# Kernel tuning notes

Measured on AMD Instinct MI355X. Metric: run time of the kernel, lower is better.

The kernel has to match this reference:

```python
import jax, jax.numpy as jnp
import numpy as np

B, LQ, NK, D, H, FF, NL = 32, 96, 2048, 384, 8, 1536, 6
DH = D // H
NFUT = 32
GOAL_S, GRASP_S = 2046, 2047  # goal=[2046,2047), grasp=[2047,2048) in k_cross and k_self


def rotary3d(xyz):
    # RotaryPositionEncoding3D: per-axis sinusoids, interleaved duplication, concat over x/y/z
    d3 = D // 3
    div = jnp.exp(jnp.arange(0, d3, 2, dtype=jnp.float32) * (-np.log(10000.0) / d3))  # [d3/2]
    ang = xyz[..., None] * div  # [B,N,3,d3/2]
    cos = jnp.repeat(jnp.cos(ang), 2, axis=-1)  # [B,N,3,d3] (f0,f0,f1,f1,...)
    sin = jnp.repeat(jnp.sin(ang), 2, axis=-1)
    b, n = xyz.shape[:2]
    return cos.reshape(b, n, D), sin.reshape(b, n, D)


def rope(x, cos, sin):
    x2 = jnp.stack([-x[..., 1::2], x[..., ::2]], axis=-1).reshape(x.shape)
    return x * cos + x2 * sin


def layernorm(x, g, b):
    m = jnp.mean(x, -1, keepdims=True)
    v = jnp.var(x, -1, keepdims=True)
    return (x - m) * jax.lax.rsqrt(v + 1e-5) * g + b


def attn_block(x, kv, qcos, qsin, kcos, ksin, t_feats, p):
    (aw, ab, wq_, bq_, wk_, bk_, wv_, bv_, wo_, bo_, g1, b1, fw1_, fb1_, fw2_, fb2_, g2, b2_) = p
    # AdaLN: time-conditioned scale/shift on the query stream
    mod = jax.nn.silu(t_feats) @ aw + ab  # [B,2D]
    scale, shift = jnp.split(mod, 2, axis=-1)
    xq = x * (1.0 + scale[:, None, :]) + shift[:, None, :]
    qp = rope(xq @ wq_ + bq_, qcos, qsin).reshape(B, -1, H, DH)
    kp = rope(kv @ wk_ + bk_, kcos, ksin).reshape(B, -1, H, DH)
    vp = (kv @ wv_ + bv_).reshape(B, -1, H, DH)
    att = jax.nn.softmax(jnp.einsum('bqhd,bkhd->bhqk', qp, kp) / np.sqrt(DH), axis=-1)
    o = jnp.einsum('bhqk,bkhd->bqhd', att, vp).reshape(B, -1, D) @ wo_ + bo_
    x = layernorm(x + o, g1, b1)  # post-norm (pre_norm=False), residual on un-modulated x
    f = jax.nn.relu(x @ fw1_ + fb1_) @ fw2_ + fb2_
    return layernorm(x + f, g2, b2_)


def mlp_head(x, w1, b1, w2, b2, w3, b3):
    h = jax.nn.relu(x @ w1 + b1)
    h = jax.nn.relu(h @ w2 + b2)
    return h @ w3 + b3


def _forward(q, k_cross, k_self, q_xyz, k_xyz, timesteps,
             t_w1, t_b1, t_w2, t_b2, type_emb,
             ada_w, ada_b, wq, bq, wk, bk, wv, bv, wo, bo,
             ln1_g, ln1_b, fw1, fb1, fw2, fb2, ln2_g, ln2_b,
             act_w1, act_b1, act_w2, act_b2, act_w3, act_b3,
             qf_w1, qf_b1, qf_w2, qf_b2, qf_w3, qf_b3,
             ob_w1, ob_b1, ob_w2, ob_b2, ob_w3, ob_b3):
    # SinusoidalPosEmb + MLP time embedding
    half = D // 2
    freqs = jnp.exp(jnp.arange(half, dtype=jnp.float32) * (-np.log(10000.0) / (half - 1)))
    a = timesteps[:, None] * freqs
    pe = jnp.concatenate([jnp.sin(a), jnp.cos(a)], axis=-1)
    t_feats = jax.nn.relu(pe @ t_w1 + t_b1) @ t_w2 + t_b2  # [B,D]

    qcos, qsin = rotary3d(q_xyz)
    kcos, ksin = rotary3d(k_xyz)
    scos = jnp.concatenate([kcos, qcos], axis=1)  # self layers: seq2_pos = cat(pcd, grasp)
    ssin = jnp.concatenate([ksin, qsin], axis=1)

    # type embeddings (conditions_only -> goal=id3, grasp=id4)
    kc = k_cross.at[:, GOAL_S:GOAL_S + 1].add(type_emb[3]).at[:, GRASP_S:GRASP_S + 1].add(type_emb[4])
    ksf = k_self.at[:, GOAL_S:GOAL_S + 1].add(type_emb[3]).at[:, GRASP_S:GRASP_S + 1].add(type_emb[4])

    x = q
    for i in range(NL):
        p = (ada_w[i], ada_b[i], wq[i], bq[i], wk[i], bk[i], wv[i], bv[i], wo[i], bo[i],
             ln1_g[i], ln1_b[i], fw1[i], fb1[i], fw2[i], fb2[i], ln2_g[i], ln2_b[i])
        if i < 2:  # cross_attn module (2 layers) over scene tokens
            x = attn_block(x, kc, qcos, qsin, kcos, ksin, t_feats, p)
        else:      # 4 shared attention layers over k_self
            x = attn_block(x, ksf, qcos, qsin, scos, ssin, t_feats, p)

    act = mlp_head(x[:, :NFUT], act_w1, act_b1, act_w2, act_b2, act_w3, act_b3)            # [B,32,31]
    qf = mlp_head(x[:, NFUT:2 * NFUT], qf_w1, qf_b1, qf_w2, qf_b2, qf_w3, qf_b3)           # [B,32,31]
    ob = mlp_head(x[:, 2 * NFUT:], ob_w1, ob_b1, ob_w2, ob_b2, ob_w3, ob_b3)               # [B,32,9]
    return jnp.concatenate([act, qf, ob], axis=-1)  # [B,32,71]


def setup_inputs():
    ks = iter(jax.random.split(jax.random.key(0), 80))
    def w(shape, s=0.02):
        return jax.random.normal(next(ks), shape, jnp.float32) * s
    inp = {
        'q': jax.random.normal(next(ks), (B, LQ, D), jnp.float32),
        'k_cross': jax.random.normal(next(ks), (B, NK, D), jnp.float32),
        'k_self': jax.random.normal(next(ks), (B, NK + LQ, D), jnp.float32),
        'q_xyz': jax.random.normal(next(ks), (B, LQ, 3), jnp.float32),
        'k_xyz': jax.random.normal(next(ks), (B, NK, 3), jnp.float32),
        'timesteps': jax.random.uniform(next(ks), (B,), jnp.float32) * 1000.0,
        't_w1': w((D, D)), 't_b1': jnp.zeros((D,)), 't_w2': w((D, D)), 't_b2': jnp.zeros((D,)),
        'type_emb': w((8, D)),
        'ada_w': w((NL, D, 2 * D)), 'ada_b': jnp.zeros((NL, 2 * D)),
        'wq': w((NL, D, D)), 'bq': jnp.zeros((NL, D)),
        'wk': w((NL, D, D)), 'bk': jnp.zeros((NL, D)),
        'wv': w((NL, D, D)), 'bv': jnp.zeros((NL, D)),
        'wo': w((NL, D, D)), 'bo': jnp.zeros((NL, D)),
        'ln1_g': jnp.ones((NL, D)), 'ln1_b': jnp.zeros((NL, D)),
        'fw1': w((NL, D, FF)), 'fb1': jnp.zeros((NL, FF)),
        'fw2': w((NL, FF, D)), 'fb2': jnp.zeros((NL, D)),
        'ln2_g': jnp.ones((NL, D)), 'ln2_b': jnp.zeros((NL, D)),
        'act_w1': w((D, D)), 'act_b1': jnp.zeros((D,)), 'act_w2': w((D, D)), 'act_b2': jnp.zeros((D,)),
        'act_w3': w((D, 31)), 'act_b3': jnp.zeros((31,)),
        'qf_w1': w((D, D)), 'qf_b1': jnp.zeros((D,)), 'qf_w2': w((D, D)), 'qf_b2': jnp.zeros((D,)),
        'qf_w3': w((D, 31)), 'qf_b3': jnp.zeros((31,)),
        'ob_w1': w((D, D)), 'ob_b1': jnp.zeros((D,)), 'ob_w2': w((D, D)), 'ob_b2': jnp.zeros((D,)),
        'ob_w3': w((D, 9)), 'ob_b3': jnp.zeros((9,)),
    }
    return inp


def reference(q, k_cross, k_self, q_xyz, k_xyz, timesteps,
              t_w1, t_b1, t_w2, t_b2, type_emb,
              ada_w, ada_b, wq, bq, wk, bk, wv, bv, wo, bo,
              ln1_g, ln1_b, fw1, fb1, fw2, fb2, ln2_g, ln2_b,
              act_w1, act_b1, act_w2, act_b2, act_w3, act_b3,
              qf_w1, qf_b1, qf_w2, qf_b2, qf_w3, qf_b3,
              ob_w1, ob_b1, ob_w2, ob_b2, ob_w3, ob_b3):
    return _forward(q, k_cross, k_self, q_xyz, k_xyz, timesteps,
                    t_w1, t_b1, t_w2, t_b2, type_emb,
                    ada_w, ada_b, wq, bq, wk, bk, wv, bv, wo, bo,
                    ln1_g, ln1_b, fw1, fb1, fw2, fb2, ln2_g, ln2_b,
                    act_w1, act_b1, act_w2, act_b2, act_w3, act_b3,
                    qf_w1, qf_b1, qf_w2, qf_b2, qf_w3, qf_b3,
                    ob_w1, ob_b1, ob_w2, ob_b2, ob_w3, ob_b3)
```

## Files before the change

kernel.cpp:

```cpp
#include <hip/hip_runtime.h>
#include <hip/hip_fp16.h>

#define B_   32
#define LQ_  96
#define NK_  2048
#define D_   384
#define H_   8
#define DH_  48
#define FF_  1536
#define MQ_  (B_*LQ_)
#define SATT 8

typedef float  f32x4  __attribute__((ext_vector_type(4)));
typedef __bf16 bf16x8 __attribute__((ext_vector_type(8)));

__device__ __forceinline__ unsigned short f2bf(float f) {
  union { float f; unsigned u; } v; v.f = f;
  unsigned r = v.u + 0x7fffu + ((v.u >> 16) & 1u);
  return (unsigned short)(r >> 16);
}

__device__ __forceinline__ void ld_g2l(const unsigned short* g, unsigned short* l) {
  __builtin_amdgcn_global_load_lds(
      (const __attribute__((address_space(1))) void*)g,
      (__attribute__((address_space(3))) void*)l, 16, 0, 0);
}

__global__ void time_embed_kernel(const float* __restrict__ ts,
                                  const float* __restrict__ w1, const float* __restrict__ b1,
                                  const float* __restrict__ w2, const float* __restrict__ b2,
                                  float* __restrict__ s_out) {
  int b = blockIdx.x, d = threadIdx.x;
  __shared__ float pe[384];
  __shared__ float h1[384];
  float t = ts[b];
  int dd = (d < 192) ? d : d - 192;
  float f = expf((float)dd * (-9.210340371976184f / 191.0f));
  float ang = t * f;
  pe[d] = (d < 192) ? sinf(ang) : cosf(ang);
  __syncthreads();
  float acc = b1[d];
  for (int k = 0; k < 384; ++k) acc += pe[k] * w1[k * 384 + d];
  h1[d] = fmaxf(acc, 0.f);
  __syncthreads();
  acc = b2[d];
  for (int k = 0; k < 384; ++k) acc += h1[k] * w2[k * 384 + d];
  s_out[b * 384 + d] = acc / (1.f + expf(-acc));
}

__global__ void adaln_mod_kernel(const float* __restrict__ s,
                                 const float* __restrict__ aw, const float* __restrict__ ab,
                                 float* __restrict__ mod) {
  int b = blockIdx.x, l = blockIdx.y, c = threadIdx.x;
  __shared__ float ss[384];
  if (c < 384) ss[c] = s[b * 384 + c];
  __syncthreads();
  float acc = ab[l * 768 + c];
  const float* w = aw + (long)l * 384 * 768;
  for (int k = 0; k < 384; ++k) acc += ss[k] * w[k * 768 + c];
  mod[((long)l * 32 + b) * 768 + c] = acc;
}

__global__ void rope_pack_kernel(const float* __restrict__ xyz, __half2* __restrict__ cs,
                                 int total, int N, int ldn, int noff) {
  for (int i = blockIdx.x * blockDim.x + threadIdx.x; i < total;
       i += gridDim.x * blockDim.x) {
    int p = i % 192;
    int n = (i / 192) % N;
    int b = i / (192 * N);
    int a = p >> 6, j = p & 63;
    float div = __expf((float)j * (-9.210340371976184f / 64.0f));
    float ang = xyz[((long)b * N + n) * 3 + a] * div;
    float sv, cv;
    __sincosf(ang, &sv, &cv);
    cs[((long)b * ldn + noff + n) * 192 + p] = __floats2half2_rn(cv, sv);
  }
}

__global__ void cast_type_kernel(const float* __restrict__ in, const float* __restrict__ temb,
                                 unsigned short* __restrict__ out, long total, int N) {
  for (long i = blockIdx.x * (long)blockDim.x + threadIdx.x; i < total;
       i += (long)gridDim.x * blockDim.x) {
    int d = (int)(i % 384);
    int n = (int)((i / 384) % N);
    float v = in[i];
    if (n == 2046) v += temb[3 * 384 + d];
    else if (n == 2047) v += temb[4 * 384 + d];
    out[i] = f2bf(v);
  }
}

__global__ void wtrans_kernel(const float* __restrict__ in, unsigned short* __restrict__ out,
                              long total, int K, int N, int LDN, int noff) {
  for (long i = blockIdx.x * (long)blockDim.x + threadIdx.x; i < total;
       i += (long)gridDim.x * blockDim.x) {
    long l = i / ((long)K * N);
    long rem = i - l * (long)K * N;
    int n = (int)(rem / K);
    int k = (int)(rem % K);
    out[(l * LDN + noff + n) * K + k] = f2bf(in[l * (long)K * N + (long)k * N + n]);
  }
}

__global__ void modx_kernel(const float* __restrict__ x, const float* __restrict__ modl,
                            unsigned short* __restrict__ xq) {
  int i = blockIdx.x * blockDim.x + threadIdx.x;
  if (i >= MQ_ * D_) return;
  int d = i % 384;
  int b = (i / 384) / 96;
  float sc = modl[b * 768 + d];
  float sh = modl[b * 768 + 384 + d];
  xq[i] = f2bf(x[i] * (1.f + sc) + sh);
}

#define EPI_RELU   1
#define EPI_F32    2
#define EPI_ROPE_Q 3
#define EPI_KV     4

template <int EPI, int TM, int XT, int PERM>
__global__ __launch_bounds__(256)
void gemm_bt(const unsigned short* __restrict__ A, const unsigned short* __restrict__ Bt,
             const float* __restrict__ biasK, const float* __restrict__ biasV,
             void* __restrict__ Cout, void* __restrict__ Cout2,
             int Nt, int K, const __half2* __restrict__ cs, int tabOff, int nPerRow) {
  __shared__ __align__(16) unsigned short As[3][TM * 32];
  __shared__ __align__(16) unsigned short Bs[3][128 * 32];
  int tid = threadIdx.x, lane = tid & 63, wid = tid >> 6;
  int wm = (wid >> 1) * (TM / 2), wn = (wid & 1) * 64;
  int bx, byi;
  if (XT > 0) {
    int id = blockIdx.x;
    int xcd = id & 7, slot = id >> 3;
    bx = slot % XT;
    byi = (slot / XT) * 8 + xcd;
  } else {
    bx = blockIdx.x; byi = blockIdx.y;
  }
  int bn = bx * 128;
  long bm = (long)byi * TM;
  int r0 = tid >> 2;
  int cg = ((tid & 3) + (tid >> 3)) & 3;
  int c0 = cg * 8;
  long ar0 = bm + r0, ar1 = bm + 64 + r0;
  if (PERM) {
    ar0 = (ar0 >> 5) * 96 + tabOff + (ar0 & 31);
    ar1 = (ar1 >> 5) * 96 + tabOff + (ar1 & 31);
  }
  const unsigned short* gA0 = A + ar0 * K + c0;
  const unsigned short* gA1 = A + ar1 * K + c0;
  const unsigned short* gB0 = Bt + (long)(bn + r0) * K + c0;
  const unsigned short* gB1 = Bt + (long)(bn + 64 + r0) * K + c0;
  f32x4 acc[TM / 32][4] = {};
  int nk = K >> 5;
  int la = lane & 15, lg8 = lane >> 4;
  auto stage = [&](int buf) {
    ld_g2l(gA0, &As[buf][tid * 8]);
    if (TM == 128) ld_g2l(gA1, &As[buf][2048 + tid * 8]);
    ld_g2l(gB0, &Bs[buf][tid * 8]);
    ld_g2l(gB1, &Bs[buf][2048 + tid * 8]);
    gA0 += 32; gA1 += 32; gB0 += 32; gB1 += 32;
  };
  int offA[TM / 32], offB[4];
#pragma unroll
  for (int i = 0; i < TM / 32; ++i) {
    int row = wm + i * 16 + la;
    offA[i] = row * 32 + ((lg8 - (row >> 1)) & 3) * 8;
  }
#pragma unroll
  for (int j = 0; j < 4; ++j) {
    int row = wn + j * 16 + la;
    offB[j] = row * 32 + ((lg8 - (row >> 1)) & 3) * 8;
  }
  stage(0);
  stage(1);
  for (int kc = 0; kc < nk; ++kc) {
    int cur = kc % 3;
    if (kc < nk - 1) {
      if (TM == 128) asm volatile("s_waitcnt vmcnt(4) lgkmcnt(0)" ::: "memory");
      else           asm volatile("s_waitcnt vmcnt(3) lgkmcnt(0)" ::: "memory");
    } else {
      asm volatile("s_waitcnt vmcnt(0) lgkmcnt(0)" ::: "memory");
    }
    asm volatile("s_barrier" ::: "memory");
    if (kc + 2 < nk) stage((kc + 2) % 3);
    const unsigned short* Ab = &As[cur][0];
    const unsigned short* Bb = &Bs[cur][0];
    bf16x8 af[TM / 32], bfr[4];
#pragma unroll
    for (int i = 0; i < TM / 32; ++i) af[i] = *(const bf16x8*)&Ab[offA[i]];
#pragma unroll
    for (int j = 0; j < 4; ++j) bfr[j] = *(const bf16x8*)&Bb[offB[j]];
#pragma unroll
    for (int i = 0; i < TM / 32; ++i)
#pragma unroll
      for (int j = 0; j < 4; ++j)
        acc[i][j] = __builtin_amdgcn_mfma_f32_16x16x32_bf16(af[i], bfr[j], acc[i][j], 0, 0, 0);
  }
  int lr = lg8 * 4;
  const float SCALE = 0.14433756729740643f;
  bool isV = false;
  const float* bptr = biasK;
  if (EPI == EPI_KV) { isV = (bn >= 384); if (isV) bptr = biasV - 384; }
#pragma unroll
  for (int i = 0; i < TM / 32; ++i) {
#pragma unroll
    for (int r = 0; r < 4; ++r) {
      int row = (int)bm + wm + i * 16 + lr + r;
      int bb = 0, nn = 0; long ti = 0;
      if (EPI == EPI_ROPE_Q || EPI == EPI_KV) {
        bb = row / nPerRow;
        nn = row - bb * nPerRow;
        ti = ((long)bb * 2144 + tabOff + nn) * 192;
      }
#pragma unroll
      for (int j = 0; j < 4; ++j) {
        int col = bn + wn + j * 16 + la;
        float v = acc[i][j][r] + bptr[col];
        if (EPI == EPI_F32) {
          ((float*)Cout)[(long)row * Nt + col] = v;
        } else if (EPI == EPI_RELU) {
          ((unsigned short*)Cout)[(long)row * Nt + col] = f2bf(fmaxf(v, 0.f));
        } else if (EPI == EPI_KV && isV) {
          ((unsigned short*)Cout2)[(long)row * 384 + (col - 384)] = f2bf(v);
        } else {
          float pv = __shfl_xor(v, 1);
          int p = ((col >> 7) << 6) + ((col & 127) >> 1);
          __half2 hv = cs[ti + p];
          float cc = __low2float(hv), ssv = __high2float(hv);
          float o = (col & 1) ? (v * cc + pv * ssv) : (v * cc - pv * ssv);
          if (EPI == EPI_ROPE_Q) {
            ((unsigned short*)Cout)[(long)row * Nt + col] = f2bf(o * SCALE);
          } else {
            int h = col / 48, d = col - h * 48;
            ((unsigned short*)Cout)[((long)((bb << 3) + h) * nPerRow + nn) * 48 + d] = f2bf(o);
          }
        }
      }
    }
  }
}

__global__ __launch_bounds__(384)
void attn_part_kernel(const unsigned short* __restrict__ Q, const unsigned short* __restrict__ Kg,
                      const unsigned short* __restrict__ Vrm, float* __restrict__ Opart,
                      float* __restrict__ Lpart, int N, int S) {
  int h = blockIdx.x, b = blockIdx.y, s = blockIdx.z;
  int bh = b * 8 + h;
  int tid = threadIdx.x, lane = tid & 63, w = tid >> 6;
  __shared__ __align__(16) unsigned short Qs[96][64];
  __shared__ __align__(16) unsigned short Ks[2][32][72];
  __shared__ __align__(16) unsigned short Vst[2][64][40];
  __shared__ __align__(16) unsigned short Ps[6][16][40];
  const uint4 z4 = {0u, 0u, 0u, 0u};
  for (int e = tid; e < 576; e += 384) {
    int row = e / 6, g = e % 6;
    *(uint4*)&Qs[row][g * 8] = *(const uint4*)&Q[((long)b * 96 + row) * 384 + h * 48 + g * 8];
  }
  for (int e = tid; e < 192; e += 384) {
    int row = e >> 1, g = e & 1;
    *(uint4*)&Qs[row][48 + g * 8] = z4;
  }
  if (tid < 192) {
    int pb = tid / 96, rr = (tid % 96) / 3, g = tid % 3;
    *(uint4*)&Ks[pb][rr][48 + g * 8] = z4;
  }
  if (tid < 150) {
    int pb = tid / 75, e = tid % 75;
    *(uint4*)(&Vst[pb][49][0] + e * 8) = z4;
  }
  if (tid < 80) {
    int pb = tid / 40, c = tid % 40;
    Vst[pb][48][c] = (c < 32) ? (unsigned short)0x3F80 : (unsigned short)0;
  }
  __syncthreads();
  int la = lane & 15, lg = (lane >> 4) * 8;
  bf16x8 qf0 = *(const bf16x8*)&Qs[w * 16 + la][lg];
  bf16x8 qf1 = *(const bf16x8*)&Qs[w * 16 + la][32 + lg];
  f32x4 of[4] = {};
  int ntile = N >> 5;
  int t0 = (s * ntile) / S, t1 = ((s + 1) * ntile) / S;
  int stt = (tid < 192) ? tid : tid - 192;
  int krow = stt / 6, kg = stt % 6;
  const uint4* gsrc = (tid < 192)
      ? (const uint4*)(Kg + ((long)bh * N + krow) * 48 + kg * 8)
      : (const uint4*)(Vrm + ((long)b * N + krow) * 384 + h * 48 + kg * 8);
  int tstep = (tid < 192) ? 192 : 1536;
  uint4 pref = gsrc[(long)t0 * tstep];
  for (int it = t0; it < t1; ++it) {
    int p = it & 1;
    if (tid < 192) {
      *(uint4*)&Ks[p][krow][kg * 8] = pref;
    } else {
      union { uint4 q; unsigned short u[8]; } t; t.q = pref;
#pragma unroll
      for (int e = 0; e < 8; ++e) {
        int ee = (e + kg) & 7;
        Vst[p][kg * 8 + ee][krow] = t.u[ee];
      }
    }
    asm volatile("s_waitcnt lgkmcnt(0)" ::: "memory");
    asm volatile("s_barrier" ::: "memory");
    if (it + 1 < t1) pref = gsrc[(long)(it + 1) * tstep];
    f32x4 sc[2] = {};
#pragma unroll
    for (int ctile = 0; ctile < 2; ++ctile) {
      bf16x8 kf0 = *(const bf16x8*)&Ks[p][ctile * 16 + la][lg];
      bf16x8 kf1 = *(const bf16x8*)&Ks[p][ctile * 16 + la][32 + lg];
      sc[ctile] = __builtin_amdgcn_mfma_f32_16x16x32_bf16(qf0, kf0, sc[ctile], 0, 0, 0);
      sc[ctile] = __builtin_amdgcn_mfma_f32_16x16x32_bf16(qf1, kf1, sc[ctile], 0, 0, 0);
    }
    int prow = (lane >> 4) * 4;
#pragma unroll
    for (int ctile = 0; ctile < 2; ++ctile)
#pragma unroll
      for (int r = 0; r < 4; ++r)
        Ps[w][prow + r][ctile * 16 + la] = f2bf(__expf(sc[ctile][r]));
    asm volatile("s_waitcnt lgkmcnt(0)" ::: "memory");
    bf16x8 pf = *(const bf16x8*)&Ps[w][la][lg];
#pragma unroll
    for (int dt = 0; dt < 4; ++dt) {
      bf16x8 vf = *(const bf16x8*)&Vst[p][dt * 16 + la][lg];
      of[dt] = __builtin_amdgcn_mfma_f32_16x16x32_bf16(pf, vf, of[dt], 0, 0, 0);
    }
  }
  long base = ((long)s * 256 + bh) * 96;
#pragma unroll
  for (int r = 0; r < 4; ++r) {
    int qrow = w * 16 + (lane >> 4) * 4 + r;
    float L = __shfl(of[3][r], lane & 48);
#pragma unroll
    for (int dt = 0; dt < 3; ++dt)
      Opart[(base + qrow) * 48 + dt * 16 + la] = of[dt][r];
    if (la == 0) Lpart[base + qrow] = L;
  }
}

__global__ __launch_bounds__(384)
void attn_combine_kernel(const float* __restrict__ Opart, const float* __restrict__ Lpart,
                         unsigned short* __restrict__ O, int S) {
  int h = blockIdx.x, b = blockIdx.y;
  int bh = b * 8 + h;
  for (int e = threadIdx.x; e < 96 * 48; e += 384) {
    int q = e / 48, d = e % 48;
    float L = 0.f, acc = 0.f;
    for (int s = 0; s < S; ++s) {
      long ib = ((long)s * 256 + bh) * 96 + q;
      L += Lpart[ib];
      acc += Opart[ib * 48 + d];
    }
    O[((long)b * 96 + q) * 384 + h * 48 + d] = f2bf(acc / L);
  }
}

__global__ __launch_bounds__(128)
void ln_res_kernel(const float* __restrict__ xin, const float* __restrict__ delta,
                   const float* __restrict__ g, const float* __restrict__ bt,
                   const float* __restrict__ modl,
                   float* __restrict__ xout, unsigned short* __restrict__ xbf,
                   unsigned short* __restrict__ xqb) {
  int row = blockIdx.x, tid = threadIdx.x;
  __shared__ float red[128];
  float v[3];
#pragma unroll
  for (int i = 0; i < 3; ++i) {
    int d = tid + i * 128;
    v[i] = xin[(long)row * 384 + d] + delta[(long)row * 384 + d];
  }
  red[tid] = v[0] + v[1] + v[2];
  __syncthreads();
  for (int t = 64; t > 0; t >>= 1) { if (tid < t) red[tid] += red[tid + t]; __syncthreads(); }
  float mean = red[0] / 384.f;
  __syncthreads();
  float q = 0.f;
#pragma unroll
  for (int i = 0; i < 3; ++i) { float d0 = v[i] - mean; q += d0 * d0; }
  red[tid] = q;
  __syncthreads();
  for (int t = 64; t > 0; t >>= 1) { if (tid < t) red[tid] += red[tid + t]; __syncthreads(); }
  float rstd = rsqrtf(red[0] / 384.f + 1e-5f);
  int bb = row / 96;
#pragma unroll
  for (int i = 0; i < 3; ++i) {
    int d = tid + i * 128;
    float o = (v[i] - mean) * rstd * g[d] + bt[d];
    xout[(long)row * 384 + d] = o;
    xbf[(long)row * 384 + d] = f2bf(o);
    if (modl) {
      float sc = modl[bb * 768 + d];
      float sh = modl[bb * 768 + 384 + d];
      xqb[(long)row * 384 + d] = f2bf(o * (1.f + sc) + sh);
    }
  }
}

__global__ __launch_bounds__(64)
void rowgemm_bf(const unsigned short* __restrict__ A, const float* __restrict__ W,
                const float* __restrict__ bias, float* __restrict__ out,
                int Nc, int ooff) {
  int r = blockIdx.x, tid = threadIdx.x;
  __shared__ float as[384];
  for (int k = tid; k < 384; k += 64) {
    union { unsigned u; float f; } c; c.u = (unsigned)A[(long)r * 384 + k] << 16;
    as[k] = c.f;
  }
  __syncthreads();
  if (tid < Nc) {
    float acc = bias[tid];
    for (int k = 0; k < 384; ++k) acc += as[k] * W[k * Nc + tid];
    out[(long)r * 71 + ooff + tid] = acc;
  }
}

extern "C" void kernel_launch(void* const* d_in, const int* in_sizes, int n_in,
                              void* d_out, int out_size, void* d_ws, size_t ws_size,
                              hipStream_t stream) {
  const float* q_in    = (const float*)d_in[0];
  const float* k_cross = (const float*)d_in[1];
  const float* k_self  = (const float*)d_in[2];
  const float* q_xyz   = (const float*)d_in[3];
  const float* k_xyz   = (const float*)d_in[4];
  const float* tsteps  = (const float*)d_in[5];
  const float* t_w1 = (const float*)d_in[6];
  const float* t_b1 = (const float*)d_in[7];
  const float* t_w2 = (const float*)d_in[8];
  const float* t_b2 = (const float*)d_in[9];
  const float* type_emb = (const float*)d_in[10];
  const float* ada_w = (const float*)d_in[11];
  const float* ada_b = (const float*)d_in[12];
  const float* wq = (const float*)d_in[13]; const float* bq = (const float*)d_in[14];
  const float* wk = (const float*)d_in[15]; const float* bk = (const float*)d_in[16];
  const float* wv = (const float*)d_in[17]; const float* bv = (const float*)d_in[18];
  const float* wo = (const float*)d_in[19]; const float* bo = (const float*)d_in[20];
  const float* ln1g = (const float*)d_in[21]; const float* ln1b = (const float*)d_in[22];
  const float* fw1 = (const float*)d_in[23]; const float* fb1 = (const float*)d_in[24];
  const float* fw2 = (const float*)d_in[25]; const float* fb2 = (const float*)d_in[26];
  const float* ln2g = (const float*)d_in[27]; const float* ln2b = (const float*)d_in[28];
  const float* hw[9]; const float* hb[9];
  for (int i = 0; i < 9; ++i) { hw[i] = (const float*)d_in[29 + 2 * i]; hb[i] = (const float*)d_in[30 + 2 * i]; }

  char* ws = (char*)d_ws;
  size_t off = 0;
  auto alloc = [&](size_t bytes) -> void* {
    void* p = ws + off;
    off += (bytes + 255) & ~(size_t)255;
    return p;
  };
  float* s_silu = (float*)alloc((size_t)32 * 384 * 4);
  float* mod    = (float*)alloc((size_t)6 * 32 * 768 * 4);
  __half2* cs_all = (__half2*)alloc((size_t)32 * 2144 * 192 * 4);
  unsigned short* kcb  = (unsigned short*)alloc((size_t)32 * 2048 * 384 * 2);
  unsigned short* ksb  = (unsigned short*)alloc((size_t)32 * 2144 * 384 * 2);
  unsigned short* wqt  = (unsigned short*)alloc((size_t)6 * 384 * 384 * 2);
  unsigned short* wkvt = (unsigned short*)alloc((size_t)6 * 768 * 384 * 2);
  unsigned short* wot  = (unsigned short*)alloc((size_t)6 * 384 * 384 * 2);
  unsigned short* fw1t = (unsigned short*)alloc((size_t)6 * 384 * 1536 * 2);
  unsigned short* fw2t = (unsigned short*)alloc((size_t)6 * 384 * 1536 * 2);
  unsigned short* hwt  = (unsigned short*)alloc((size_t)6 * 384 * 384 * 2);
  float* x            = (float*)alloc((size_t)MQ_ * 384 * 4);
  unsigned short* xbf  = (unsigned short*)alloc((size_t)MQ_ * 384 * 2);
  unsigned short* xqb  = (unsigned short*)alloc((size_t)MQ_ * 384 * 2);
  unsigned short* qrope= (unsigned short*)alloc((size_t)MQ_ * 384 * 2);
  unsigned short* Kc   = (unsigned short*)alloc((size_t)256 * 2144 * 48 * 2);
  unsigned short* Vrm  = (unsigned short*)alloc((size_t)32 * 2144 * 384 * 2);
  unsigned short* aout = (unsigned short*)alloc((size_t)MQ_ * 384 * 2);
  float* tmp          = (float*)alloc((size_t)MQ_ * 384 * 4);
  unsigned short* ffh  = (unsigned short*)alloc((size_t)MQ_ * 1536 * 2);
  unsigned short* hh1  = (unsigned short*)alloc((size_t)1024 * 384 * 2);
  unsigned short* hh2  = (unsigned short*)alloc((size_t)1024 * 384 * 2);
  float* Opart        = (float*)alloc((size_t)SATT * 256 * 96 * 48 * 4);
  float* Lpart        = (float*)alloc((size_t)SATT * 256 * 96 * 4);
  (void)ws_size; (void)in_sizes; (void)n_in; (void)out_size;

  time_embed_kernel<<<32, 384, 0, stream>>>(tsteps, t_w1, t_b1, t_w2, t_b2, s_silu);
  adaln_mod_kernel<<<dim3(32, 6), 768, 0, stream>>>(s_silu, ada_w, ada_b, mod);
  rope_pack_kernel<<<4096, 256, 0, stream>>>(k_xyz, cs_all, 32 * 2048 * 192, 2048, 2144, 0);
  rope_pack_kernel<<<1024, 256, 0, stream>>>(q_xyz, cs_all, 32 * 96 * 192, 96, 2144, 2048);
  cast_type_kernel<<<4096, 256, 0, stream>>>(k_cross, type_emb, kcb, (long)32 * 2048 * 384, 2048);
  cast_type_kernel<<<4096, 256, 0, stream>>>(k_self, type_emb, ksb, (long)32 * 2144 * 384, 2144);
  wtrans_kernel<<<1024, 256, 0, stream>>>(wq, wqt, (long)6 * 384 * 384, 384, 384, 384, 0);
  wtrans_kernel<<<1024, 256, 0, stream>>>(wk, wkvt, (long)6 * 384 * 384, 384, 384, 768, 0);
  wtrans_kernel<<<1024, 256, 0, stream>>>(wv, wkvt, (long)6 * 384 * 384, 384, 384, 768, 384);
  wtrans_kernel<<<1024, 256, 0, stream>>>(wo, wot, (long)6 * 384 * 384, 384, 384, 384, 0);
  wtrans_kernel<<<2048, 256, 0, stream>>>(fw1, fw1t, (long)6 * 384 * 1536, 384, 1536, 1536, 0);
  wtrans_kernel<<<2048, 256, 0, stream>>>(fw2, fw2t, (long)6 * 1536 * 384, 1536, 384, 384, 0);
  for (int hd = 0; hd < 3; ++hd) {
    wtrans_kernel<<<256, 256, 0, stream>>>(hw[hd * 3 + 0], hwt + (long)(hd * 2) * 384 * 384,
                                           (long)384 * 384, 384, 384, 384, 0);
    wtrans_kernel<<<256, 256, 0, stream>>>(hw[hd * 3 + 1], hwt + (long)(hd * 2 + 1) * 384 * 384,
                                           (long)384 * 384, 384, 384, 384, 0);
  }
  hipMemcpyAsync(x, q_in, (size_t)MQ_ * 384 * 4, hipMemcpyDeviceToDevice, stream);
  modx_kernel<<<(MQ_ * 384 + 255) / 256, 256, 0, stream>>>(x, mod, xqb);

  for (int l = 0; l < 6; ++l) {
    int Nl = (l < 2) ? 2048 : 2144;
    const unsigned short* kvsrc = (l < 2) ? kcb : ksb;
    gemm_bt<EPI_ROPE_Q, 64, 0, 0><<<dim3(3, 48), 256, 0, stream>>>(
        xqb, wqt + (long)l * 384 * 384, bq + l * 384, nullptr, qrope, nullptr,
        384, 384, cs_all, 2048, 96);
    gemm_bt<EPI_KV, 128, 6, 0><<<dim3(6 * (32 * Nl / 128)), 256, 0, stream>>>(
        kvsrc, wkvt + (long)l * 768 * 384, bk + l * 384, bv + l * 384, Kc, Vrm,
        768, 384, cs_all, 0, Nl);
    attn_part_kernel<<<dim3(8, 32, SATT), 384, 0, stream>>>(qrope, Kc, Vrm, Opart, Lpart, Nl, SATT);
    attn_combine_kernel<<<dim3(8, 32), 384, 0, stream>>>(Opart, Lpart, aout, SATT);
    gemm_bt<EPI_F32, 64, 0, 0><<<dim3(3, 48), 256, 0, stream>>>(
        aout, wot + (long)l * 384 * 384, bo + l * 384, nullptr, tmp, nullptr,
        384, 384, nullptr, 0, 96);
    ln_res_kernel<<<MQ_, 128, 0, stream>>>(x, tmp, ln1g + l * 384, ln1b + l * 384,
                                           nullptr, x, xbf, nullptr);
    gemm_bt<EPI_RELU, 128, 0, 0><<<dim3(12, 24), 256, 0, stream>>>(
        xbf, fw1t + (long)l * 1536 * 384, fb1 + l * 1536, nullptr, ffh, nullptr,
        1536, 384, nullptr, 0, 96);
    gemm_bt<EPI_F32, 64, 0, 0><<<dim3(3, 48), 256, 0, stream>>>(
        ffh, fw2t + (long)l * 384 * 1536, fb2 + l * 384, nullptr, tmp, nullptr,
        384, 1536, nullptr, 0, 96);
    ln_res_kernel<<<MQ_, 128, 0, stream>>>(x, tmp, ln2g + l * 384, ln2b + l * 384,
                                           (l < 5) ? (mod + (long)(l + 1) * 32 * 768) : nullptr,
                                           x, xbf, xqb);
  }

  const int ooffs[3] = {0, 31, 62};
  const int nouts[3] = {31, 31, 9};
  for (int hd = 0; hd < 3; ++hd) {
    gemm_bt<EPI_RELU, 64, 0, 1><<<dim3(3, 16), 256, 0, stream>>>(
        xbf, hwt + (long)(hd * 2) * 384 * 384, hb[hd * 3 + 0], nullptr, hh1, nullptr,
        384, 384, nullptr, hd * 32, 96);
    gemm_bt<EPI_RELU, 64, 0, 0><<<dim3(3, 16), 256, 0, stream>>>(
        hh1, hwt + (long)(hd * 2 + 1) * 384 * 384, hb[hd * 3 + 1], nullptr, hh2, nullptr,
        384, 384, nullptr, 0, 96);
    rowgemm_bf<<<1024, 64, 0, stream>>>(hh2, hw[hd * 3 + 2], hb[hd * 3 + 2], (float*)d_out,
                                        nouts[hd], ooffs[hd]);
  }
}
```

Measured before the change: 2.426 ms.

## Move RoPE from GEMM epilogues into attention loads and widen GEMM K-tile

```diff
diff --git a/kernel.cpp b/kernel.cpp
--- a/kernel.cpp
+++ b/kernel.cpp
@@ -19,11 +19,28 @@
   unsigned r = v.u + 0x7fffu + ((v.u >> 16) & 1u);
   return (unsigned short)(r >> 16);
 }
+__device__ __forceinline__ float bf2f(unsigned short u) {
+  union { unsigned u; float f; } c; c.u = (unsigned)u << 16;
+  return c.f;
+}
 
 __device__ __forceinline__ void ld_g2l(const unsigned short* g, unsigned short* l) {
   __builtin_amdgcn_global_load_lds(
       (const __attribute__((address_space(1))) void*)g,
       (__attribute__((address_space(3))) void*)l, 16, 0, 0);
+}
+
+__device__ __forceinline__ uint4 rope8(uint4 raw, uint4 tab, float scale) {
+  union { uint4 q; unsigned short u[8]; } in, out; in.q = raw;
+  union { uint4 q; __half2 h[4]; } t; t.q = tab;
+#pragma unroll
+  for (int i = 0; i < 4; ++i) {
+    float lo = bf2f(in.u[2 * i]), hi = bf2f(in.u[2 * i + 1]);
+    float c = __low2float(t.h[i]), s = __high2float(t.h[i]);
+    out.u[2 * i]     = f2bf((lo * c - hi * s) * scale);
+    out.u[2 * i + 1] = f2bf((hi * c + lo * s) * scale);
+  }
+  return out.q;
 }
 
 __global__ void time_embed_kernel(const float* __restrict__ ts,
@@ -113,19 +130,17 @@
   xq[i] = f2bf(x[i] * (1.f + sc) + sh);
 }
 
+#define EPI_BF16   0
 #define EPI_RELU   1
 #define EPI_F32    2
-#define EPI_ROPE_Q 3
-#define EPI_KV     4
 
 template <int EPI, int TM, int XT, int PERM>
 __global__ __launch_bounds__(256)
 void gemm_bt(const unsigned short* __restrict__ A, const unsigned short* __restrict__ Bt,
              const float* __restrict__ biasK, const float* __restrict__ biasV,
-             void* __restrict__ Cout, void* __restrict__ Cout2,
-             int Nt, int K, const __half2* __restrict__ cs, int tabOff, int nPerRow) {
-  __shared__ __align__(16) unsigned short As[3][TM * 32];
-  __shared__ __align__(16) unsigned short Bs[3][128 * 32];
+             void* __restrict__ Cout, int Nt, int K, int permOff) {
+  __shared__ __align__(16) unsigned short As[2][TM * 64];
+  __shared__ __align__(16) unsigned short Bs[2][128 * 64];
   int tid = threadIdx.x, lane = tid & 63, wid = tid >> 6;
   int wm = (wid >> 1) * (TM / 2), wn = (wid & 1) * 64;
   int bx, byi;
@@ -139,111 +154,88 @@
   }
   int bn = bx * 128;
   long bm = (long)byi * TM;
-  int r0 = tid >> 2;
-  int cg = ((tid & 3) + (tid >> 3)) & 3;
-  int c0 = cg * 8;
-  long ar0 = bm + r0, ar1 = bm + 64 + r0;
-  if (PERM) {
-    ar0 = (ar0 >> 5) * 96 + tabOff + (ar0 & 31);
-    ar1 = (ar1 >> 5) * 96 + tabOff + (ar1 & 31);
-  }
-  const unsigned short* gA0 = A + ar0 * K + c0;
-  const unsigned short* gA1 = A + ar1 * K + c0;
-  const unsigned short* gB0 = Bt + (long)(bn + r0) * K + c0;
-  const unsigned short* gB1 = Bt + (long)(bn + 64 + r0) * K + c0;
+  int t8 = tid >> 3;
+  int cg = ((tid & 7) + t8) & 7;
+  const unsigned short* gAc[TM / 32];
+#pragma unroll
+  for (int c = 0; c < TM / 32; ++c) {
+    long ar = bm + c * 32 + t8;
+    if (PERM) ar = (ar >> 5) * 96 + permOff + (ar & 31);
+    gAc[c] = A + ar * K + cg * 8;
+  }
+  const unsigned short* gB = Bt + (long)(bn + t8) * K + cg * 8;
   f32x4 acc[TM / 32][4] = {};
-  int nk = K >> 5;
+  int nk = K >> 6;
   int la = lane & 15, lg8 = lane >> 4;
   auto stage = [&](int buf) {
-    ld_g2l(gA0, &As[buf][tid * 8]);
-    if (TM == 128) ld_g2l(gA1, &As[buf][2048 + tid * 8]);
-    ld_g2l(gB0, &Bs[buf][tid * 8]);
-    ld_g2l(gB1, &Bs[buf][2048 + tid * 8]);
-    gA0 += 32; gA1 += 32; gB0 += 32; gB1 += 32;
+    unsigned short* Ad = &As[buf][0];
+    unsigned short* Bd = &Bs[buf][0];
+#pragma unroll
+    for (int c = 0; c < TM / 32; ++c) { ld_g2l(gAc[c], Ad + c * 2048 + tid * 8); gAc[c] += 64; }
+#pragma unroll
+    for (int c = 0; c < 4; ++c) ld_g2l(gB + (long)c * 32 * K, Bd + c * 2048 + tid * 8);
+    gB += 64;
   };
-  int offA[TM / 32], offB[4];
+  int offA[TM / 32][2], offB[4][2];
 #pragma unroll
   for (int i = 0; i < TM / 32; ++i) {
     int row = wm + i * 16 + la;
-    offA[i] = row * 32 + ((lg8 - (row >> 1)) & 3) * 8;
+#pragma unroll
+    for (int ks = 0; ks < 2; ++ks)
+      offA[i][ks] = row * 64 + (((ks * 4 + lg8) - row) & 7) * 8;
   }
 #pragma unroll
   for (int j = 0; j < 4; ++j) {
     int row = wn + j * 16 + la;
-    offB[j] = row * 32 + ((lg8 - (row >> 1)) & 3) * 8;
+#pragma unroll
+    for (int ks = 0; ks < 2; ++ks)
+      offB[j][ks] = row * 64 + (((ks * 4 + lg8) - row) & 7) * 8;
   }
   stage(0);
-  stage(1);
   for (int kc = 0; kc < nk; ++kc) {
-    int cur = kc % 3;
-    if (kc < nk - 1) {
-      if (TM == 128) asm volatile("s_waitcnt vmcnt(4) lgkmcnt(0)" ::: "memory");
-      else           asm volatile("s_waitcnt vmcnt(3) lgkmcnt(0)" ::: "memory");
-    } else {
-      asm volatile("s_waitcnt vmcnt(0) lgkmcnt(0)" ::: "memory");
-    }
+    int cur = kc & 1;
+    asm volatile("s_waitcnt vmcnt(0) lgkmcnt(0)" ::: "memory");
     asm volatile("s_barrier" ::: "memory");
-    if (kc + 2 < nk) stage((kc + 2) % 3);
+    if (kc + 1 < nk) stage(cur ^ 1);
     const unsigned short* Ab = &As[cur][0];
     const unsigned short* Bb = &Bs[cur][0];
-    bf16x8 af[TM / 32], bfr[4];
-#pragma unroll
-    for (int i = 0; i < TM / 32; ++i) af[i] = *(const bf16x8*)&Ab[offA[i]];
-#pragma unroll
-    for (int j = 0; j < 4; ++j) bfr[j] = *(const bf16x8*)&Bb[offB[j]];
-#pragma unroll
-    for (int i = 0; i < TM / 32; ++i)
-#pragma unroll
-      for (int j = 0; j < 4; ++j)
-        acc[i][j] = __builtin_amdgcn_mfma_f32_16x16x32_bf16(af[i], bfr[j], acc[i][j], 0, 0, 0);
+#pragma unroll
+    for (int ks = 0; ks < 2; ++ks) {
+      bf16x8 af[TM / 32], bfr[4];
+#pragma unroll
+      for (int i = 0; i < TM / 32; ++i) af[i] = *(const bf16x8*)&Ab[offA[i][ks]];
+#pragma unroll
+      for (int j = 0; j < 4; ++j) bfr[j] = *(const bf16x8*)&Bb[offB[j][ks]];
+#pragma unroll
+      for (int i = 0; i < TM / 32; ++i)
+#pragma unroll
+        for (int j = 0; j < 4; ++j)
+          acc[i][j] = __builtin_amdgcn_mfma_f32_16x16x32_bf16(af[i], bfr[j], acc[i][j], 0, 0, 0);
+    }
   }
   int lr = lg8 * 4;
-  const float SCALE = 0.14433756729740643f;
-  bool isV = false;
   const float* bptr = biasK;
-  if (EPI == EPI_KV) { isV = (bn >= 384); if (isV) bptr = biasV - 384; }
+  if (biasV && bn >= 384) bptr = biasV - 384;
 #pragma unroll
   for (int i = 0; i < TM / 32; ++i) {
 #pragma unroll
     for (int r = 0; r < 4; ++r) {
-      int row = (int)bm + wm + i * 16 + lr + r;
-      int bb = 0, nn = 0; long ti = 0;
-      if (EPI == EPI_ROPE_Q || EPI == EPI_KV) {
-        bb = row / nPerRow;
-        nn = row - bb * nPerRow;
-        ti = ((long)bb * 2144 + tabOff + nn) * 192;
-      }
+      long row = bm + wm + i * 16 + lr + r;
 #pragma unroll
       for (int j = 0; j < 4; ++j) {
         int col = bn + wn + j * 16 + la;
         float v = acc[i][j][r] + bptr[col];
-        if (EPI == EPI_F32) {
-          ((float*)Cout)[(long)row * Nt + col] = v;
-        } else if (EPI == EPI_RELU) {
-          ((unsigned short*)Cout)[(long)row * Nt + col] = f2bf(fmaxf(v, 0.f));
-        } else if (EPI == EPI_KV && isV) {
-          ((unsigned short*)Cout2)[(long)row * 384 + (col - 384)] = f2bf(v);
-        } else {
-          float pv = __shfl_xor(v, 1);
-          int p = ((col >> 7) << 6) + ((col & 127) >> 1);
-          __half2 hv = cs[ti + p];
-          float cc = __low2float(hv), ssv = __high2float(hv);
-          float o = (col & 1) ? (v * cc + pv * ssv) : (v * cc - pv * ssv);
-          if (EPI == EPI_ROPE_Q) {
-            ((unsigned short*)Cout)[(long)row * Nt + col] = f2bf(o * SCALE);
-          } else {
-            int h = col / 48, d = col - h * 48;
-            ((unsigned short*)Cout)[((long)((bb << 3) + h) * nPerRow + nn) * 48 + d] = f2bf(o);
-          }
-        }
+        if (EPI == EPI_F32)      ((float*)Cout)[row * Nt + col] = v;
+        else if (EPI == EPI_RELU) ((unsigned short*)Cout)[row * Nt + col] = f2bf(fmaxf(v, 0.f));
+        else                      ((unsigned short*)Cout)[row * Nt + col] = f2bf(v);
       }
     }
   }
 }
 
 __global__ __launch_bounds__(384)
-void attn_part_kernel(const unsigned short* __restrict__ Q, const unsigned short* __restrict__ Kg,
-                      const unsigned short* __restrict__ Vrm, float* __restrict__ Opart,
+void attn_part_kernel(const unsigned short* __restrict__ Q, const unsigned short* __restrict__ KV,
+                      const __half2* __restrict__ cs, float* __restrict__ Opart,
                       float* __restrict__ Lpart, int N, int S) {
   int h = blockIdx.x, b = blockIdx.y, s = blockIdx.z;
   int bh = b * 8 + h;
@@ -253,9 +245,14 @@
   __shared__ __align__(16) unsigned short Vst[2][64][40];
   __shared__ __align__(16) unsigned short Ps[6][16][40];
   const uint4 z4 = {0u, 0u, 0u, 0u};
+  const float SCALE = 0.14433756729740643f;
   for (int e = tid; e < 576; e += 384) {
     int row = e / 6, g = e % 6;
-    *(uint4*)&Qs[row][g * 8] = *(const uint4*)&Q[((long)b * 96 + row) * 384 + h * 48 + g * 8];
+    int col = h * 48 + g * 8;
+    uint4 qraw = *(const uint4*)&Q[((long)b * 96 + row) * 384 + col];
+    int pb = ((col >> 7) << 6) + ((col & 127) >> 1);
+    uint4 tb = *(const uint4*)&cs[((long)b * 2144 + 2048 + row) * 192 + pb];
+    *(uint4*)&Qs[row][g * 8] = rope8(qraw, tb, SCALE);
   }
   for (int e = tid; e < 192; e += 384) {
     int row = e >> 1, g = e & 1;
@@ -282,15 +279,17 @@
   int t0 = (s * ntile) / S, t1 = ((s + 1) * ntile) / S;
   int stt = (tid < 192) ? tid : tid - 192;
   int krow = stt / 6, kg = stt % 6;
-  const uint4* gsrc = (tid < 192)
-      ? (const uint4*)(Kg + ((long)bh * N + krow) * 48 + kg * 8)
-      : (const uint4*)(Vrm + ((long)b * N + krow) * 384 + h * 48 + kg * 8);
-  int tstep = (tid < 192) ? 192 : 1536;
-  uint4 pref = gsrc[(long)t0 * tstep];
+  int colK = h * 48 + kg * 8;
+  int pbK = ((colK >> 7) << 6) + ((colK & 127) >> 1);
+  const uint4* gD = (const uint4*)(KV + ((long)b * N + krow) * 768 +
+                                   ((tid < 192) ? colK : (384 + colK)));
+  const uint4* gT = (const uint4*)(cs + ((long)b * 2144 + krow) * 192 + pbK);
+  uint4 pref = gD[(long)t0 * 3072];
+  uint4 tpref = (tid < 192) ? gT[(long)t0 * 1536] : z4;
   for (int it = t0; it < t1; ++it) {
     int p = it & 1;
     if (tid < 192) {
-      *(uint4*)&Ks[p][krow][kg * 8] = pref;
+      *(uint4*)&Ks[p][krow][kg * 8] = rope8(pref, tpref, 1.f);
     } else {
       union { uint4 q; unsigned short u[8]; } t; t.q = pref;
 #pragma unroll
@@ -301,7 +300,10 @@
     }
     asm volatile("s_waitcnt lgkmcnt(0)" ::: "memory");
     asm volatile("s_barrier" ::: "memory");
-    if (it + 1 < t1) pref = gsrc[(long)(it + 1) * tstep];
+    if (it + 1 < t1) {
+      pref = gD[(long)(it + 1) * 3072];
+      if (tid < 192) tpref = gT[(long)(it + 1) * 1536];
+    }
     f32x4 sc[2] = {};
 #pragma unroll
     for (int ctile = 0; ctile < 2; ++ctile) {
@@ -400,10 +402,7 @@
                 int Nc, int ooff) {
   int r = blockIdx.x, tid = threadIdx.x;
   __shared__ float as[384];
-  for (int k = tid; k < 384; k += 64) {
-    union { unsigned u; float f; } c; c.u = (unsigned)A[(long)r * 384 + k] << 16;
-    as[k] = c.f;
-  }
+  for (int k = tid; k < 384; k += 64) as[k] = bf2f(A[(long)r * 384 + k]);
   __syncthreads();
   if (tid < Nc) {
     float acc = bias[tid];
@@ -460,9 +459,8 @@
   float* x            = (float*)alloc((size_t)MQ_ * 384 * 4);
   unsigned short* xbf  = (unsigned short*)alloc((size_t)MQ_ * 384 * 2);
   unsigned short* xqb  = (unsigned short*)alloc((size_t)MQ_ * 384 * 2);
-  unsigned short* qrope= (unsigned short*)alloc((size_t)MQ_ * 384 * 2);
-  unsigned short* Kc   = (unsigned short*)alloc((size_t)256 * 2144 * 48 * 2);
-  unsigned short* Vrm  = (unsigned short*)alloc((size_t)32 * 2144 * 384 * 2);
+  unsigned short* qb   = (unsigned short*)alloc((size_t)MQ_ * 384 * 2);
+  unsigned short* KVb  = (unsigned short*)alloc((size_t)32 * 2144 * 768 * 2);
   unsigned short* aout = (unsigned short*)alloc((size_t)MQ_ * 384 * 2);
   float* tmp          = (float*)alloc((size_t)MQ_ * 384 * 4);
   unsigned short* ffh  = (unsigned short*)alloc((size_t)MQ_ * 1536 * 2);
@@ -496,25 +494,20 @@
   for (int l = 0; l < 6; ++l) {
     int Nl = (l < 2) ? 2048 : 2144;
     const unsigned short* kvsrc = (l < 2) ? kcb : ksb;
-    gemm_bt<EPI_ROPE_Q, 64, 0, 0><<<dim3(3, 48), 256, 0, stream>>>(
-        xqb, wqt + (long)l * 384 * 384, bq + l * 384, nullptr, qrope, nullptr,
-        384, 384, cs_all, 2048, 96);
-    gemm_bt<EPI_KV, 128, 6, 0><<<dim3(6 * (32 * Nl / 128)), 256, 0, stream>>>(
-        kvsrc, wkvt + (long)l * 768 * 384, bk + l * 384, bv + l * 384, Kc, Vrm,
-        768, 384, cs_all, 0, Nl);
-    attn_part_kernel<<<dim3(8, 32, SATT), 384, 0, stream>>>(qrope, Kc, Vrm, Opart, Lpart, Nl, SATT);
+    gemm_bt<EPI_BF16, 64, 0, 0><<<dim3(3, 48), 256, 0, stream>>>(
+        xqb, wqt + (long)l * 384 * 384, bq + l * 384, nullptr, qb, 384, 384, 0);
+    gemm_bt<EPI_BF16, 128, 6, 0><<<dim3(6 * (32 * Nl / 128)), 256, 0, stream>>>(
+        kvsrc, wkvt + (long)l * 768 * 384, bk + l * 384, bv + l * 384, KVb, 768, 384, 0);
+    attn_part_kernel<<<dim3(8, 32, SATT), 384, 0, stream>>>(qb, KVb, cs_all, Opart, Lpart, Nl, SATT);
     attn_combine_kernel<<<dim3(8, 32), 384, 0, stream>>>(Opart, Lpart, aout, SATT);
     gemm_bt<EPI_F32, 64, 0, 0><<<dim3(3, 48), 256, 0, stream>>>(
-        aout, wot + (long)l * 384 * 384, bo + l * 384, nullptr, tmp, nullptr,
-        384, 384, nullptr, 0, 96);
+        aout, wot + (long)l * 384 * 384, bo + l * 384, nullptr, tmp, 384, 384, 0);
     ln_res_kernel<<<MQ_, 128, 0, stream>>>(x, tmp, ln1g + l * 384, ln1b + l * 384,
                                            nullptr, x, xbf, nullptr);
     gemm_bt<EPI_RELU, 128, 0, 0><<<dim3(12, 24), 256, 0, stream>>>(
-        xbf, fw1t + (long)l * 1536 * 384, fb1 + l * 1536, nullptr, ffh, nullptr,
-        1536, 384, nullptr, 0, 96);
+        xbf, fw1t + (long)l * 1536 * 384, fb1 + l * 1536, nullptr, ffh, 1536, 384, 0);
     gemm_bt<EPI_F32, 64, 0, 0><<<dim3(3, 48), 256, 0, stream>>>(
-        ffh, fw2t + (long)l * 384 * 1536, fb2 + l * 384, nullptr, tmp, nullptr,
-        384, 1536, nullptr, 0, 96);
+        ffh, fw2t + (long)l * 384 * 1536, fb2 + l * 384, nullptr, tmp, 384, 1536, 0);
     ln_res_kernel<<<MQ_, 128, 0, stream>>>(x, tmp, ln2g + l * 384, ln2b + l * 384,
                                            (l < 5) ? (mod + (long)(l + 1) * 32 * 768) : nullptr,
                                            x, xbf, xqb);
@@ -524,11 +517,9 @@
   const int nouts[3] = {31, 31, 9};
   for (int hd = 0; hd < 3; ++hd) {
     gemm_bt<EPI_RELU, 64, 0, 1><<<dim3(3, 16), 256, 0, stream>>>(
-        xbf, hwt + (long)(hd * 2) * 384 * 384, hb[hd * 3 + 0], nullptr, hh1, nullptr,
-        384, 384, nullptr, hd * 32, 96);
+        xbf, hwt + (long)(hd * 2) * 384 * 384, hb[hd * 3 + 0], nullptr, hh1, 384, 384, hd * 32);
     gemm_bt<EPI_RELU, 64, 0, 0><<<dim3(3, 16), 256, 0, stream>>>(
-        hh1, hwt + (long)(hd * 2 + 1) * 384 * 384, hb[hd * 3 + 1], nullptr, hh2, nullptr,
-        384, 384, nullptr, 0, 96);
+        hh1, hwt + (long)(hd * 2 + 1) * 384 * 384, hb[hd * 3 + 1], nullptr, hh2, 384, 384, 0);
     rowgemm_bf<<<1024, 64, 0, stream>>>(hh2, hw[hd * 3 + 2], hb[hd * 3 + 2], (float*)d_out,
                                         nouts[hd], ooffs[hd]);
   }
```

New measurement: 2.120 ms. 1.14x faster.
